# Optimization experiments

Measured on AMD Instinct MI355X. Metric: run time of the kernel, lower is better.

Reference implementation:

```python
import jax, jax.numpy as jnp
import numpy as np

N_NODES = 50000
N_EDGES = 640000
DIM = 128
N_LAYERS = 4
K_MAX = 4


def setup_inputs() -> dict:
    key = jax.random.key(0)
    k1, k2, k3, k4, k5, k6 = jax.random.split(key, 6)
    x = jax.random.normal(k1, (N_NODES, DIM), dtype=jnp.float32)
    edge_index = jax.random.randint(k2, (2, N_EDGES), 0, N_NODES, dtype=jnp.int32)
    edge_attr = jax.random.randint(k3, (N_EDGES,), 1, K_MAX + 1, dtype=jnp.int32)  # hop k in [1, k_max]
    W = jax.random.normal(k4, (N_LAYERS, DIM, DIM), dtype=jnp.float32) * 0.05
    b = jax.random.normal(k5, (N_LAYERS, DIM), dtype=jnp.float32) * 0.01
    alpha = jax.random.normal(k6, (N_LAYERS, K_MAX), dtype=jnp.float32)
    return {"x": x, "edge_index": edge_index, "edge_attr": edge_attr,
            "W": W, "b": b, "alpha": alpha}


def reference(x, edge_index, edge_attr, W, b, alpha):
    # SP-GCN stage: per-hop GCN convs with shared per-layer weight W[t],
    # combined with softmax(alpha[t]) hop weights, residual + ReLU + L2 norm.
    N, D = x.shape
    L, K = alpha.shape
    src, dst = edge_index[0], edge_index[1]
    k_idx = edge_attr - 1                              # [E] in [0, K)

    # Per-(node, hop) in-degree with self-loop (+1), as in gcn_norm per k-subgraph.
    seg = dst * K + k_idx
    ones = jnp.ones(src.shape[0], dtype=x.dtype)
    deg = jax.ops.segment_sum(ones, seg, num_segments=N * K).reshape(N, K) + 1.0  # [N, K]
    dinv = jax.lax.rsqrt(deg)
    # symmetric norm per edge within its hop-k subgraph
    norm_e = dinv[src, k_idx] * dinv[dst, k_idx]       # [E]

    for t in range(L):
        a = jax.nn.softmax(alpha[t])                   # [K] hop weights
        h = x @ W[t]                                   # [N, D]
        # sum_k alpha_k * conv_k fused: per-edge weight alpha[k_e] * norm_e
        msg = (a[k_idx] * norm_e)[:, None] * h[src]    # [E, D]
        agg = jax.ops.segment_sum(msg, dst, num_segments=N)
        # self-loop contributions: sum_k alpha_k / deg[n, k]
        self_coef = jnp.sum(a[None, :] / deg, axis=1)  # [N]
        out = agg + self_coef[:, None] * h + b[t]
        x = x + jax.nn.relu(out)
        # F.normalize(p=2, dim=-1), eps=1e-12
        nrm = jnp.maximum(jnp.linalg.norm(x, axis=-1, keepdims=True), 1e-12)
        x = x / nrm
    return x
```

## Files before the change

kernel.cpp:

```cpp
#include <hip/hip_runtime.h>
#include <hip/hip_fp16.h>
#include <math.h>

#define DIM 128
#define KH 4

typedef unsigned int uint;
typedef unsigned short ushort;
using short8v = __attribute__((ext_vector_type(8))) short;
using f32x4 = __attribute__((ext_vector_type(4))) float;

__device__ __forceinline__ uint f2bf(float f) {
  uint u = __float_as_uint(f);
  return (u + 0x7fffu + ((u >> 16) & 1u)) >> 16;
}
__device__ __forceinline__ float bf2f(uint u) { return __uint_as_float(u << 16); }
__device__ __forceinline__ float bflo(uint u) { return __uint_as_float(u << 16); }
__device__ __forceinline__ float bfhi(uint u) { return __uint_as_float(u & 0xffff0000u); }

__global__ __launch_bounds__(256) void k_init(const float4* __restrict__ xin,
                                              float4* __restrict__ X4,
                                              uint* __restrict__ Xhi,
                                              uint* __restrict__ Xlo,
                                              uint* __restrict__ degpack,
                                              int n4, int N) {
  int i = blockIdx.x * 256 + threadIdx.x;
  if (i < n4) {
    float4 v = xin[i];
    X4[i] = v;
    uint h0 = f2bf(v.x), h1 = f2bf(v.y), h2 = f2bf(v.z), h3 = f2bf(v.w);
    Xhi[i * 2 + 0] = h0 | (h1 << 16);
    Xhi[i * 2 + 1] = h2 | (h3 << 16);
    uint l0 = f2bf(v.x - bf2f(h0)), l1 = f2bf(v.y - bf2f(h1));
    uint l2 = f2bf(v.z - bf2f(h2)), l3 = f2bf(v.w - bf2f(h3));
    Xlo[i * 2 + 0] = l0 | (l1 << 16);
    Xlo[i * 2 + 1] = l2 | (l3 << 16);
  }
  if (i < N) degpack[i] = 0;
}

__global__ __launch_bounds__(256) void k_wprep(const float* __restrict__ W,
                                               short* __restrict__ Whi,
                                               short* __restrict__ Wlo, int total) {
  int idx = blockIdx.x * 256 + threadIdx.x;
  if (idx >= total) return;
  int l = idx >> 14;
  int rem = idx & 16383;
  int k = rem >> 7;
  int n = rem & 127;
  float w = W[idx];
  uint h = f2bf(w);
  uint lo = f2bf(w - bf2f(h));
  size_t o = (size_t)l * 16384 + (size_t)n * 128 + k;
  Whi[o] = (short)h;
  Wlo[o] = (short)lo;
}

__global__ __launch_bounds__(256) void k_count(const int* __restrict__ ei,
                                               const int* __restrict__ attr,
                                               uint* __restrict__ degpack, int E) {
  int e = blockIdx.x * 256 + threadIdx.x;
  if (e >= E) return;
  int dst = ei[E + e];
  int k = attr[e] - 1;
  atomicAdd(&degpack[dst], 1u << (k * 8));
}

__global__ __launch_bounds__(256) void k_scan1(const uint* __restrict__ degpack,
                                               int* __restrict__ off,
                                               int* __restrict__ bsum, int n) {
  __shared__ int s[256];
  int t = threadIdx.x;
  int i = blockIdx.x * 256 + t;
  int v = 0;
  if (i < n) {
    uint w = degpack[i];
    v = (w & 0xff) + ((w >> 8) & 0xff) + ((w >> 16) & 0xff) + (w >> 24);
  }
  s[t] = v;
  __syncthreads();
  for (int d = 1; d < 256; d <<= 1) {
    int u = (t >= d) ? s[t - d] : 0;
    __syncthreads();
    s[t] += u;
    __syncthreads();
  }
  if (i < n) off[i] = s[t] - v;
  if (t == 255) bsum[blockIdx.x] = s[255];
}

__global__ __launch_bounds__(256) void k_scan2(const int* __restrict__ bsum,
                                               int* __restrict__ bex, int nb) {
  __shared__ int s[256];
  int t = threadIdx.x;
  int v = (t < nb) ? bsum[t] : 0;
  s[t] = v;
  __syncthreads();
  for (int d = 1; d < 256; d <<= 1) {
    int u = (t >= d) ? s[t - d] : 0;
    __syncthreads();
    s[t] += u;
    __syncthreads();
  }
  if (t < nb) bex[t] = s[t] - v;
}

__global__ __launch_bounds__(256) void k_scan3(int* __restrict__ off,
                                               const int* __restrict__ bex,
                                               const uint* __restrict__ degpack,
                                               int* __restrict__ cursor4,
                                               float* __restrict__ dinv, int n) {
  int i = blockIdx.x * 256 + threadIdx.x;
  if (i >= n) return;
  int o = off[i] + bex[blockIdx.x];
  off[i] = o;
  uint w = degpack[i];
  int b0 = w & 0xff, b1 = (w >> 8) & 0xff, b2 = (w >> 16) & 0xff, b3 = w >> 24;
  int4 c;
  c.x = o;
  c.y = o + b0;
  c.z = o + b0 + b1;
  c.w = o + b0 + b1 + b2;
  *(int4*)&cursor4[i * 4] = c;
  float4 dv;
  dv.x = rsqrtf((float)b0 + 1.0f);
  dv.y = rsqrtf((float)b1 + 1.0f);
  dv.z = rsqrtf((float)b2 + 1.0f);
  dv.w = rsqrtf((float)b3 + 1.0f);
  *(float4*)&dinv[i * 4] = dv;
}

__global__ __launch_bounds__(256) void k_scatter(const int* __restrict__ ei,
                                                 const int* __restrict__ attr,
                                                 const float* __restrict__ dinv,
                                                 int* __restrict__ cursor4,
                                                 uint* __restrict__ srcnm, int E) {
  int e = blockIdx.x * 256 + threadIdx.x;
  if (e >= E) return;
  int src = ei[e];
  int dst = ei[E + e];
  int k = attr[e] - 1;
  float nm = dinv[src * KH + k] * dinv[dst * KH + k];
  ushort h = __half_as_ushort(__float2half(nm));
  int pos = atomicAdd(&cursor4[dst * KH + k], 1);
  srcnm[pos] = (uint)src | ((uint)h << 16);
}

__global__ __launch_bounds__(512) void k_gemm(const uint* __restrict__ Xhi,
                                              const uint* __restrict__ Xlo,
                                              const short* __restrict__ Whi,
                                              const short* __restrict__ Wlo,
                                              ushort* __restrict__ Hb16, int N) {
  __shared__ __align__(16) short xs_hi[64 * 128];
  __shared__ __align__(16) short xs_lo[64 * 128];
  int t = threadIdx.x;
  int r0 = blockIdx.x * 64;

#pragma unroll
  for (int i = 0; i < 2; ++i) {
    int fi = i * 512 + t;
    int row = fi >> 4, kq = fi & 15;
    int rg = r0 + row;
    if (rg >= N) rg = N - 1;
    int swz = kq ^ (row & 7);
    *(uint4*)&xs_hi[row * 128 + swz * 8] = *(const uint4*)&Xhi[(size_t)rg * 64 + kq * 4];
    *(uint4*)&xs_lo[row * 128 + swz * 8] = *(const uint4*)&Xlo[(size_t)rg * 64 + kq * 4];
  }
  __syncthreads();

  int wid = t >> 6, lane = t & 63;
  int wrow = wid & 1, wcol = wid >> 1;
  int lr = lane & 15, lk = lane >> 4;

  f32x4 acc[2][2];
#pragma unroll
  for (int a = 0; a < 2; ++a)
#pragma unroll
    for (int c = 0; c < 2; ++c) acc[a][c] = (f32x4){0.f, 0.f, 0.f, 0.f};

#pragma unroll
  for (int ks = 0; ks < 4; ++ks) {
    int k0 = ks * 32 + lk * 8;
    short8v ah[2], al[2];
#pragma unroll
    for (int rt = 0; rt < 2; ++rt) {
      int r = wrow * 32 + rt * 16 + lr;
      int slot = (k0 >> 3) ^ (r & 7);
      ah[rt] = *(short8v*)&xs_hi[r * 128 + slot * 8];
      al[rt] = *(short8v*)&xs_lo[r * 128 + slot * 8];
    }
    short8v bh[2], bl[2];
#pragma unroll
    for (int ct = 0; ct < 2; ++ct) {
      int col = wcol * 32 + ct * 16 + lr;
      bh[ct] = *(const short8v*)&Whi[(size_t)col * 128 + k0];
      bl[ct] = *(const short8v*)&Wlo[(size_t)col * 128 + k0];
    }
#pragma unroll
    for (int rt = 0; rt < 2; ++rt)
#pragma unroll
      for (int ct = 0; ct < 2; ++ct) {
        acc[rt][ct] = __builtin_amdgcn_mfma_f32_16x16x32_bf16(ah[rt], bh[ct], acc[rt][ct], 0, 0, 0);
        acc[rt][ct] = __builtin_amdgcn_mfma_f32_16x16x32_bf16(al[rt], bh[ct], acc[rt][ct], 0, 0, 0);
        acc[rt][ct] = __builtin_amdgcn_mfma_f32_16x16x32_bf16(ah[rt], bl[ct], acc[rt][ct], 0, 0, 0);
      }
  }

#pragma unroll
  for (int rt = 0; rt < 2; ++rt)
#pragma unroll
    for (int ct = 0; ct < 2; ++ct) {
      int col = wcol * 32 + ct * 16 + lr;
#pragma unroll
      for (int i = 0; i < 4; ++i) {
        int row = r0 + wrow * 32 + rt * 16 + lk * 4 + i;
        if (row < N) Hb16[(size_t)row * 128 + col] = (ushort)f2bf(acc[rt][ct][i]);
      }
    }
}

__global__ __launch_bounds__(256) void k_agg(const int* __restrict__ off,
                                             const uint* __restrict__ degpack,
                                             const uint* __restrict__ srcnm,
                                             const float* __restrict__ dinv,
                                             const uint* __restrict__ Hb,
                                             const float* __restrict__ bias,
                                             const float* __restrict__ alpha,
                                             float* __restrict__ X,
                                             uint* __restrict__ Xhi,
                                             uint* __restrict__ Xlo, int N) {
  int wid = threadIdx.x >> 6;
  int lane = threadIdx.x & 63;
  int n = blockIdx.x * 4 + wid;
  if (n >= N) return;

  float a0 = alpha[0], a1 = alpha[1], a2 = alpha[2], a3 = alpha[3];
  float m = fmaxf(fmaxf(a0, a1), fmaxf(a2, a3));
  a0 = __expf(a0 - m); a1 = __expf(a1 - m); a2 = __expf(a2 - m); a3 = __expf(a3 - m);
  float is = 1.0f / (a0 + a1 + a2 + a3);
  a0 *= is; a1 *= is; a2 *= is; a3 *= is;

  uint w = degpack[n];
  int b0 = w & 0xff, b1 = (w >> 8) & 0xff, b2 = (w >> 16) & 0xff, b3 = (int)(w >> 24);
  int e0 = off[n];
  int e1 = e0 + b0 + b1 + b2 + b3;
  int k1 = e0 + b0, k2 = k1 + b1, k3 = k2 + b2;

  float accx = 0.f, accy = 0.f;

  for (int base = e0; base < e1; base += 64) {
    int cnt = min(64, e1 - base);
    int sofs = 0;
    float wc = 0.f;
    if (lane < cnt) {
      uint v = srcnm[base + lane];
      int pos = base + lane;
      int k = (pos >= k1) + (pos >= k2) + (pos >= k3);
      float ak = (k == 0) ? a0 : (k == 1) ? a1 : (k == 2) ? a2 : a3;
      wc = ak * __half2float(__ushort_as_half((ushort)(v >> 16)));
      sofs = (int)(v & 0xFFFFu) << 6;
    }
    int j = 0;
    for (; j + 4 <= cnt; j += 4) {
      int s0 = __shfl(sofs, j),     s1 = __shfl(sofs, j + 1);
      int s2 = __shfl(sofs, j + 2), s3 = __shfl(sofs, j + 3);
      float w0 = __shfl(wc, j),     w1 = __shfl(wc, j + 1);
      float w2 = __shfl(wc, j + 2), w3 = __shfl(wc, j + 3);
      uint u0 = Hb[s0 + lane];
      uint u1 = Hb[s1 + lane];
      uint u2 = Hb[s2 + lane];
      uint u3 = Hb[s3 + lane];
      accx = fmaf(w0, bflo(u0), accx); accy = fmaf(w0, bfhi(u0), accy);
      accx = fmaf(w1, bflo(u1), accx); accy = fmaf(w1, bfhi(u1), accy);
      accx = fmaf(w2, bflo(u2), accx); accy = fmaf(w2, bfhi(u2), accy);
      accx = fmaf(w3, bflo(u3), accx); accy = fmaf(w3, bfhi(u3), accy);
    }
    for (; j < cnt; ++j) {
      int sj = __shfl(sofs, j);
      float wj = __shfl(wc, j);
      uint uj = Hb[sj + lane];
      accx = fmaf(wj, bflo(uj), accx);
      accy = fmaf(wj, bfhi(uj), accy);
    }
  }

  float4 dv = *(const float4*)&dinv[n * 4];
  float sc = a0 * dv.x * dv.x + a1 * dv.y * dv.y + a2 * dv.z * dv.z + a3 * dv.w * dv.w;

  uint un = Hb[(size_t)n * 64 + lane];
  float2 bb = ((const float2*)bias)[lane];
  float2 xo = ((const float2*)X)[(size_t)n * 64 + lane];
  float o0 = accx + sc * bflo(un) + bb.x;
  float o1 = accy + sc * bfhi(un) + bb.y;
  float x0 = xo.x + fmaxf(o0, 0.f);
  float x1 = xo.y + fmaxf(o1, 0.f);

  float ss = x0 * x0 + x1 * x1;
#pragma unroll
  for (int d = 32; d; d >>= 1) ss += __shfl_xor(ss, d);
  float nrm = fmaxf(sqrtf(ss), 1e-12f);
  float inv = 1.0f / nrm;
  float y0 = x0 * inv, y1 = x1 * inv;
  ((float2*)X)[(size_t)n * 64 + lane] = make_float2(y0, y1);

  uint h0 = f2bf(y0), h1 = f2bf(y1);
  Xhi[(size_t)n * 64 + lane] = h0 | (h1 << 16);
  uint l0 = f2bf(y0 - bf2f(h0)), l1 = f2bf(y1 - bf2f(h1));
  Xlo[(size_t)n * 64 + lane] = l0 | (l1 << 16);
}

extern "C" void kernel_launch(void* const* d_in, const int* in_sizes, int n_in,
                              void* d_out, int out_size, void* d_ws, size_t ws_size,
                              hipStream_t stream) {
  const float* x = (const float*)d_in[0];
  const int* ei = (const int*)d_in[1];
  const int* attr = (const int*)d_in[2];
  const float* W = (const float*)d_in[3];
  const float* b = (const float*)d_in[4];
  const float* alpha = (const float*)d_in[5];
  float* X = (float*)d_out;

  int N = in_sizes[0] / DIM;
  int E = in_sizes[1] / 2;
  int L = in_sizes[3] / (DIM * DIM);

  char* base = (char*)d_ws;
  size_t ofs = 0;
  auto carve = [&](size_t bytes) -> void* {
    void* p = base + ofs;
    ofs = (ofs + bytes + 255) & ~(size_t)255;
    return p;
  };
  int* off = (int*)carve((size_t)(N + 1) * 4);
  int* cursor4 = (int*)carve((size_t)N * KH * 4);
  uint* degpack = (uint*)carve((size_t)N * 4);
  float* dinv = (float*)carve((size_t)N * KH * 4);
  int* bsum = (int*)carve(256 * 4);
  int* bex = (int*)carve(256 * 4);
  uint* srcnm = (uint*)carve((size_t)E * 4);
  uint* Hb = (uint*)carve((size_t)N * 64 * 4);
  uint* Xhi = (uint*)carve((size_t)N * 64 * 4);
  uint* Xlo = (uint*)carve((size_t)N * 64 * 4);
  short* Whi = (short*)carve((size_t)L * DIM * DIM * 2);
  short* Wlo = (short*)carve((size_t)L * DIM * DIM * 2);

  int n4 = N * DIM / 4;
  int nb = (N + 255) / 256;
  int wtot = L * DIM * DIM;

  k_init<<<(n4 + 255) / 256, 256, 0, stream>>>((const float4*)x, (float4*)X,
                                               Xhi, Xlo, degpack, n4, N);
  k_count<<<(E + 255) / 256, 256, 0, stream>>>(ei, attr, degpack, E);
  k_scan1<<<nb, 256, 0, stream>>>(degpack, off, bsum, N);
  k_scan2<<<1, 256, 0, stream>>>(bsum, bex, nb);
  k_scan3<<<nb, 256, 0, stream>>>(off, bex, degpack, cursor4, dinv, N);
  k_scatter<<<(E + 255) / 256, 256, 0, stream>>>(ei, attr, dinv, cursor4, srcnm, E);
  k_wprep<<<(wtot + 255) / 256, 256, 0, stream>>>(W, Whi, Wlo, wtot);

  for (int t = 0; t < L; ++t) {
    k_gemm<<<(N + 63) / 64, 512, 0, stream>>>(Xhi, Xlo,
                                              Whi + (size_t)t * DIM * DIM,
                                              Wlo + (size_t)t * DIM * DIM,
                                              (ushort*)Hb, N);
    k_agg<<<(N + 3) / 4, 256, 0, stream>>>(off, degpack, srcnm, dinv, Hb,
                                           b + (size_t)t * DIM, alpha + (size_t)t * KH,
                                           X, Xhi, Xlo, N);
  }
}
```

Before: 318.4 us.

## Fuse aggregation, GEMM and normalization into one per-layer kernel

Reorders each layer to aggregate first and multiply second, (A·X)·W instead of A·(X·W). Aggregation, the split-bf16 MFMA GEMM and the residual/ReLU/L2-normalize now run in one kernel per layer that keeps the intermediate rows in shared memory, with fp16 copies of X used for the neighbor gathers. Setup kernels are also merged (init+count, scan3+weight prep), a memset is used, and X buffers ping-pong between layers. This removes the Hb round trip to global memory and one launch per layer. In exchange, 512-thread blocks each gather 64 rows serially (8 per wave), which may lower latency hiding, and fp16 gathers change numerical precision.

```diff
diff --git a/kernel.cpp b/kernel.cpp
--- a/kernel.cpp
+++ b/kernel.cpp
@@ -15,55 +15,21 @@
   return (u + 0x7fffu + ((u >> 16) & 1u)) >> 16;
 }
 __device__ __forceinline__ float bf2f(uint u) { return __uint_as_float(u << 16); }
-__device__ __forceinline__ float bflo(uint u) { return __uint_as_float(u << 16); }
-__device__ __forceinline__ float bfhi(uint u) { return __uint_as_float(u & 0xffff0000u); }
-
-__global__ __launch_bounds__(256) void k_init(const float4* __restrict__ xin,
-                                              float4* __restrict__ X4,
-                                              uint* __restrict__ Xhi,
-                                              uint* __restrict__ Xlo,
-                                              uint* __restrict__ degpack,
-                                              int n4, int N) {
+
+__global__ __launch_bounds__(256) void k_init_count(
+    const float2* __restrict__ xin, __half2* __restrict__ Xf16,
+    const int* __restrict__ ei, const int* __restrict__ attr,
+    uint* __restrict__ degpack, int n2, int E) {
   int i = blockIdx.x * 256 + threadIdx.x;
-  if (i < n4) {
-    float4 v = xin[i];
-    X4[i] = v;
-    uint h0 = f2bf(v.x), h1 = f2bf(v.y), h2 = f2bf(v.z), h3 = f2bf(v.w);
-    Xhi[i * 2 + 0] = h0 | (h1 << 16);
-    Xhi[i * 2 + 1] = h2 | (h3 << 16);
-    uint l0 = f2bf(v.x - bf2f(h0)), l1 = f2bf(v.y - bf2f(h1));
-    uint l2 = f2bf(v.z - bf2f(h2)), l3 = f2bf(v.w - bf2f(h3));
-    Xlo[i * 2 + 0] = l0 | (l1 << 16);
-    Xlo[i * 2 + 1] = l2 | (l3 << 16);
-  }
-  if (i < N) degpack[i] = 0;
-}
-
-__global__ __launch_bounds__(256) void k_wprep(const float* __restrict__ W,
-                                               short* __restrict__ Whi,
-                                               short* __restrict__ Wlo, int total) {
-  int idx = blockIdx.x * 256 + threadIdx.x;
-  if (idx >= total) return;
-  int l = idx >> 14;
-  int rem = idx & 16383;
-  int k = rem >> 7;
-  int n = rem & 127;
-  float w = W[idx];
-  uint h = f2bf(w);
-  uint lo = f2bf(w - bf2f(h));
-  size_t o = (size_t)l * 16384 + (size_t)n * 128 + k;
-  Whi[o] = (short)h;
-  Wlo[o] = (short)lo;
-}
-
-__global__ __launch_bounds__(256) void k_count(const int* __restrict__ ei,
-                                               const int* __restrict__ attr,
-                                               uint* __restrict__ degpack, int E) {
-  int e = blockIdx.x * 256 + threadIdx.x;
-  if (e >= E) return;
-  int dst = ei[E + e];
-  int k = attr[e] - 1;
-  atomicAdd(&degpack[dst], 1u << (k * 8));
+  if (i < n2) {
+    float2 v = xin[i];
+    Xf16[i] = __floats2half2_rn(v.x, v.y);
+  }
+  if (i < E) {
+    int dst = ei[E + i];
+    int k = attr[i] - 1;
+    atomicAdd(&degpack[dst], 1u << (k * 8));
+  }
 }
 
 __global__ __launch_bounds__(256) void k_scan1(const uint* __restrict__ degpack,
@@ -105,29 +71,45 @@
   if (t < nb) bex[t] = s[t] - v;
 }
 
-__global__ __launch_bounds__(256) void k_scan3(int* __restrict__ off,
-                                               const int* __restrict__ bex,
-                                               const uint* __restrict__ degpack,
-                                               int* __restrict__ cursor4,
-                                               float* __restrict__ dinv, int n) {
+__global__ __launch_bounds__(256) void k_scan3w(int* __restrict__ off,
+                                                const int* __restrict__ bex,
+                                                const uint* __restrict__ degpack,
+                                                int* __restrict__ cursor4,
+                                                float* __restrict__ dinv, int n,
+                                                const float* __restrict__ W,
+                                                short* __restrict__ Whi,
+                                                short* __restrict__ Wlo, int wtot) {
   int i = blockIdx.x * 256 + threadIdx.x;
-  if (i >= n) return;
-  int o = off[i] + bex[blockIdx.x];
-  off[i] = o;
-  uint w = degpack[i];
-  int b0 = w & 0xff, b1 = (w >> 8) & 0xff, b2 = (w >> 16) & 0xff, b3 = w >> 24;
-  int4 c;
-  c.x = o;
-  c.y = o + b0;
-  c.z = o + b0 + b1;
-  c.w = o + b0 + b1 + b2;
-  *(int4*)&cursor4[i * 4] = c;
-  float4 dv;
-  dv.x = rsqrtf((float)b0 + 1.0f);
-  dv.y = rsqrtf((float)b1 + 1.0f);
-  dv.z = rsqrtf((float)b2 + 1.0f);
-  dv.w = rsqrtf((float)b3 + 1.0f);
-  *(float4*)&dinv[i * 4] = dv;
+  if (i < n) {
+    int o = off[i] + bex[blockIdx.x];
+    off[i] = o;
+    uint w = degpack[i];
+    int b0 = w & 0xff, b1 = (w >> 8) & 0xff, b2 = (w >> 16) & 0xff, b3 = w >> 24;
+    int4 c;
+    c.x = o;
+    c.y = o + b0;
+    c.z = o + b0 + b1;
+    c.w = o + b0 + b1 + b2;
+    *(int4*)&cursor4[i * 4] = c;
+    float4 dv;
+    dv.x = rsqrtf((float)b0 + 1.0f);
+    dv.y = rsqrtf((float)b1 + 1.0f);
+    dv.z = rsqrtf((float)b2 + 1.0f);
+    dv.w = rsqrtf((float)b3 + 1.0f);
+    *(float4*)&dinv[i * 4] = dv;
+  }
+  if (i < wtot) {
+    int l = i >> 14;
+    int rem = i & 16383;
+    int k = rem >> 7;
+    int ncol = rem & 127;
+    float w = W[i];
+    uint h = f2bf(w);
+    uint lo = f2bf(w - bf2f(h));
+    size_t o = (size_t)l * 16384 + (size_t)ncol * 128 + k;
+    Whi[o] = (short)h;
+    Wlo[o] = (short)lo;
+  }
 }
 
 __global__ __launch_bounds__(256) void k_scatter(const int* __restrict__ ei,
@@ -146,32 +128,100 @@
   srcnm[pos] = (uint)src | ((uint)h << 16);
 }
 
-__global__ __launch_bounds__(512) void k_gemm(const uint* __restrict__ Xhi,
-                                              const uint* __restrict__ Xlo,
-                                              const short* __restrict__ Whi,
-                                              const short* __restrict__ Wlo,
-                                              ushort* __restrict__ Hb16, int N) {
-  __shared__ __align__(16) short xs_hi[64 * 128];
-  __shared__ __align__(16) short xs_lo[64 * 128];
+__device__ __forceinline__ void split8(f32x4 va, f32x4 vb, short8v& h, short8v& l) {
+#pragma unroll
+  for (int j = 0; j < 8; ++j) {
+    float v = (j < 4) ? va[j] : vb[j - 4];
+    uint hh = f2bf(v);
+    h[j] = (short)hh;
+    l[j] = (short)f2bf(v - bf2f(hh));
+  }
+}
+
+__global__ __launch_bounds__(512) void k_layer(
+    const int* __restrict__ off, const uint* __restrict__ degpack,
+    const uint* __restrict__ srcnm, const float* __restrict__ dinv,
+    const float2* __restrict__ Xin,
+    const __half2* __restrict__ Xf16_in,
+    const short* __restrict__ Whi, const short* __restrict__ Wlo,
+    const float* __restrict__ bias, const float* __restrict__ alpha,
+    float2* __restrict__ Xout,
+    __half2* __restrict__ Xf16_out,
+    int N) {
+  __shared__ __align__(16) char aggb[64 * 512];
   int t = threadIdx.x;
+  int wid = t >> 6, lane = t & 63;
   int r0 = blockIdx.x * 64;
 
-#pragma unroll
-  for (int i = 0; i < 2; ++i) {
-    int fi = i * 512 + t;
-    int row = fi >> 4, kq = fi & 15;
-    int rg = r0 + row;
-    if (rg >= N) rg = N - 1;
-    int swz = kq ^ (row & 7);
-    *(uint4*)&xs_hi[row * 128 + swz * 8] = *(const uint4*)&Xhi[(size_t)rg * 64 + kq * 4];
-    *(uint4*)&xs_lo[row * 128 + swz * 8] = *(const uint4*)&Xlo[(size_t)rg * 64 + kq * 4];
-  }
-  __syncthreads();
-
-  int wid = t >> 6, lane = t & 63;
+  float a0 = alpha[0], a1 = alpha[1], a2 = alpha[2], a3 = alpha[3];
+  float m = fmaxf(fmaxf(a0, a1), fmaxf(a2, a3));
+  a0 = __expf(a0 - m); a1 = __expf(a1 - m); a2 = __expf(a2 - m); a3 = __expf(a3 - m);
+  float is = 1.0f / (a0 + a1 + a2 + a3);
+  a0 *= is; a1 *= is; a2 *= is; a3 *= is;
+
+  float2 xsave[8];
+
+  for (int ni = 0; ni < 8; ++ni) {
+    int row = wid * 8 + ni;
+    int n = r0 + row;
+    if (n >= N) n = N - 1;
+    uint w = degpack[n];
+    int b0 = w & 0xff, b1 = (w >> 8) & 0xff, b2 = (w >> 16) & 0xff, b3 = (int)(w >> 24);
+    int e0 = off[n];
+    int e1 = e0 + b0 + b1 + b2 + b3;
+    int k1 = e0 + b0, k2 = k1 + b1, k3 = k2 + b2;
+    float accx = 0.f, accy = 0.f;
+
+    for (int base = e0; base < e1; base += 64) {
+      int cnt = min(64, e1 - base);
+      int sofs = 0;
+      float wc = 0.f;
+      if (lane < cnt) {
+        uint v = srcnm[base + lane];
+        int pos = base + lane;
+        int k = (pos >= k1) + (pos >= k2) + (pos >= k3);
+        float ak = (k == 0) ? a0 : (k == 1) ? a1 : (k == 2) ? a2 : a3;
+        wc = ak * __half2float(__ushort_as_half((ushort)(v >> 16)));
+        sofs = (int)(v & 0xFFFFu) << 6;
+      }
+      int j = 0;
+      for (; j + 4 <= cnt; j += 4) {
+        int s0 = __shfl(sofs, j),     s1 = __shfl(sofs, j + 1);
+        int s2 = __shfl(sofs, j + 2), s3 = __shfl(sofs, j + 3);
+        float w0 = __shfl(wc, j),     w1 = __shfl(wc, j + 1);
+        float w2 = __shfl(wc, j + 2), w3 = __shfl(wc, j + 3);
+        float2 f0 = __half22float2(Xf16_in[s0 + lane]);
+        float2 f1 = __half22float2(Xf16_in[s1 + lane]);
+        float2 f2 = __half22float2(Xf16_in[s2 + lane]);
+        float2 f3 = __half22float2(Xf16_in[s3 + lane]);
+        accx = fmaf(w0, f0.x, accx); accy = fmaf(w0, f0.y, accy);
+        accx = fmaf(w1, f1.x, accx); accy = fmaf(w1, f1.y, accy);
+        accx = fmaf(w2, f2.x, accx); accy = fmaf(w2, f2.y, accy);
+        accx = fmaf(w3, f3.x, accx); accy = fmaf(w3, f3.y, accy);
+      }
+      for (; j < cnt; ++j) {
+        int sj = __shfl(sofs, j);
+        float wj = __shfl(wc, j);
+        float2 fj = __half22float2(Xf16_in[sj + lane]);
+        accx = fmaf(wj, fj.x, accx);
+        accy = fmaf(wj, fj.y, accy);
+      }
+    }
+
+    float4 dv = *(const float4*)&dinv[n * 4];
+    float sc = a0 * dv.x * dv.x + a1 * dv.y * dv.y + a2 * dv.z * dv.z + a3 * dv.w * dv.w;
+    float2 xn = Xin[(size_t)n * 64 + lane];
+    xsave[ni] = xn;
+    accx = fmaf(sc, xn.x, accx);
+    accy = fmaf(sc, xn.y, accy);
+
+    int slot = (lane >> 1) ^ ((row & 7) << 1);
+    *(float2*)(aggb + row * 512 + slot * 16 + (lane & 1) * 8) = make_float2(accx, accy);
+  }
+  __syncthreads();
+
   int wrow = wid & 1, wcol = wid >> 1;
   int lr = lane & 15, lk = lane >> 4;
-
   f32x4 acc[2][2];
 #pragma unroll
   for (int a = 0; a < 2; ++a)
@@ -185,9 +235,10 @@
 #pragma unroll
     for (int rt = 0; rt < 2; ++rt) {
       int r = wrow * 32 + rt * 16 + lr;
-      int slot = (k0 >> 3) ^ (r & 7);
-      ah[rt] = *(short8v*)&xs_hi[r * 128 + slot * 8];
-      al[rt] = *(short8v*)&xs_lo[r * 128 + slot * 8];
+      int s0 = (k0 >> 2) ^ ((r & 7) << 1);
+      f32x4 va = *(f32x4*)(aggb + r * 512 + s0 * 16);
+      f32x4 vb = *(f32x4*)(aggb + r * 512 + s0 * 16 + 16);
+      split8(va, vb, ah[rt], al[rt]);
     }
     short8v bh[2], bl[2];
 #pragma unroll
@@ -205,6 +256,7 @@
         acc[rt][ct] = __builtin_amdgcn_mfma_f32_16x16x32_bf16(ah[rt], bl[ct], acc[rt][ct], 0, 0, 0);
       }
   }
+  __syncthreads();
 
 #pragma unroll
   for (int rt = 0; rt < 2; ++rt)
@@ -213,100 +265,30 @@
       int col = wcol * 32 + ct * 16 + lr;
 #pragma unroll
       for (int i = 0; i < 4; ++i) {
-        int row = r0 + wrow * 32 + rt * 16 + lk * 4 + i;
-        if (row < N) Hb16[(size_t)row * 128 + col] = (ushort)f2bf(acc[rt][ct][i]);
+        int row = wrow * 32 + rt * 16 + lk * 4 + i;
+        int slot = (col >> 2) ^ ((row & 7) << 1);
+        *(float*)(aggb + row * 512 + slot * 16 + (col & 3) * 4) = acc[rt][ct][i];
       }
     }
-}
-
-__global__ __launch_bounds__(256) void k_agg(const int* __restrict__ off,
-                                             const uint* __restrict__ degpack,
-                                             const uint* __restrict__ srcnm,
-                                             const float* __restrict__ dinv,
-                                             const uint* __restrict__ Hb,
-                                             const float* __restrict__ bias,
-                                             const float* __restrict__ alpha,
-                                             float* __restrict__ X,
-                                             uint* __restrict__ Xhi,
-                                             uint* __restrict__ Xlo, int N) {
-  int wid = threadIdx.x >> 6;
-  int lane = threadIdx.x & 63;
-  int n = blockIdx.x * 4 + wid;
-  if (n >= N) return;
-
-  float a0 = alpha[0], a1 = alpha[1], a2 = alpha[2], a3 = alpha[3];
-  float m = fmaxf(fmaxf(a0, a1), fmaxf(a2, a3));
-  a0 = __expf(a0 - m); a1 = __expf(a1 - m); a2 = __expf(a2 - m); a3 = __expf(a3 - m);
-  float is = 1.0f / (a0 + a1 + a2 + a3);
-  a0 *= is; a1 *= is; a2 *= is; a3 *= is;
-
-  uint w = degpack[n];
-  int b0 = w & 0xff, b1 = (w >> 8) & 0xff, b2 = (w >> 16) & 0xff, b3 = (int)(w >> 24);
-  int e0 = off[n];
-  int e1 = e0 + b0 + b1 + b2 + b3;
-  int k1 = e0 + b0, k2 = k1 + b1, k3 = k2 + b2;
-
-  float accx = 0.f, accy = 0.f;
-
-  for (int base = e0; base < e1; base += 64) {
-    int cnt = min(64, e1 - base);
-    int sofs = 0;
-    float wc = 0.f;
-    if (lane < cnt) {
-      uint v = srcnm[base + lane];
-      int pos = base + lane;
-      int k = (pos >= k1) + (pos >= k2) + (pos >= k3);
-      float ak = (k == 0) ? a0 : (k == 1) ? a1 : (k == 2) ? a2 : a3;
-      wc = ak * __half2float(__ushort_as_half((ushort)(v >> 16)));
-      sofs = (int)(v & 0xFFFFu) << 6;
-    }
-    int j = 0;
-    for (; j + 4 <= cnt; j += 4) {
-      int s0 = __shfl(sofs, j),     s1 = __shfl(sofs, j + 1);
-      int s2 = __shfl(sofs, j + 2), s3 = __shfl(sofs, j + 3);
-      float w0 = __shfl(wc, j),     w1 = __shfl(wc, j + 1);
-      float w2 = __shfl(wc, j + 2), w3 = __shfl(wc, j + 3);
-      uint u0 = Hb[s0 + lane];
-      uint u1 = Hb[s1 + lane];
-      uint u2 = Hb[s2 + lane];
-      uint u3 = Hb[s3 + lane];
-      accx = fmaf(w0, bflo(u0), accx); accy = fmaf(w0, bfhi(u0), accy);
-      accx = fmaf(w1, bflo(u1), accx); accy = fmaf(w1, bfhi(u1), accy);
-      accx = fmaf(w2, bflo(u2), accx); accy = fmaf(w2, bfhi(u2), accy);
-      accx = fmaf(w3, bflo(u3), accx); accy = fmaf(w3, bfhi(u3), accy);
-    }
-    for (; j < cnt; ++j) {
-      int sj = __shfl(sofs, j);
-      float wj = __shfl(wc, j);
-      uint uj = Hb[sj + lane];
-      accx = fmaf(wj, bflo(uj), accx);
-      accy = fmaf(wj, bfhi(uj), accy);
-    }
-  }
-
-  float4 dv = *(const float4*)&dinv[n * 4];
-  float sc = a0 * dv.x * dv.x + a1 * dv.y * dv.y + a2 * dv.z * dv.z + a3 * dv.w * dv.w;
-
-  uint un = Hb[(size_t)n * 64 + lane];
+  __syncthreads();
+
   float2 bb = ((const float2*)bias)[lane];
-  float2 xo = ((const float2*)X)[(size_t)n * 64 + lane];
-  float o0 = accx + sc * bflo(un) + bb.x;
-  float o1 = accy + sc * bfhi(un) + bb.y;
-  float x0 = xo.x + fmaxf(o0, 0.f);
-  float x1 = xo.y + fmaxf(o1, 0.f);
-
-  float ss = x0 * x0 + x1 * x1;
-#pragma unroll
-  for (int d = 32; d; d >>= 1) ss += __shfl_xor(ss, d);
-  float nrm = fmaxf(sqrtf(ss), 1e-12f);
-  float inv = 1.0f / nrm;
-  float y0 = x0 * inv, y1 = x1 * inv;
-  ((float2*)X)[(size_t)n * 64 + lane] = make_float2(y0, y1);
-
-  uint h0 = f2bf(y0), h1 = f2bf(y1);
-  Xhi[(size_t)n * 64 + lane] = h0 | (h1 << 16);
-  uint l0 = f2bf(y0 - bf2f(h0)), l1 = f2bf(y1 - bf2f(h1));
-  Xlo[(size_t)n * 64 + lane] = l0 | (l1 << 16);
+  for (int ni = 0; ni < 8; ++ni) {
+    int row = wid * 8 + ni;
+    int n = r0 + row;
+    if (n >= N) continue;
+    int slot = (lane >> 1) ^ ((row & 7) << 1);
+    float2 o = *(float2*)(aggb + row * 512 + slot * 16 + (lane & 1) * 8);
+    float x0 = xsave[ni].x + fmaxf(o.x + bb.x, 0.f);
+    float x1 = xsave[ni].y + fmaxf(o.y + bb.y, 0.f);
+    float ss = x0 * x0 + x1 * x1;
+#pragma unroll
+    for (int d = 32; d; d >>= 1) ss += __shfl_xor(ss, d);
+    float inv = 1.0f / fmaxf(sqrtf(ss), 1e-12f);
+    float y0 = x0 * inv, y1 = x1 * inv;
+    Xout[(size_t)n * 64 + lane] = make_float2(y0, y1);
+    Xf16_out[(size_t)n * 64 + lane] = __floats2half2_rn(y0, y1);
+  }
 }
 
 extern "C" void kernel_launch(void* const* d_in, const int* in_sizes, int n_in,
@@ -338,32 +320,40 @@
   int* bsum = (int*)carve(256 * 4);
   int* bex = (int*)carve(256 * 4);
   uint* srcnm = (uint*)carve((size_t)E * 4);
-  uint* Hb = (uint*)carve((size_t)N * 64 * 4);
-  uint* Xhi = (uint*)carve((size_t)N * 64 * 4);
-  uint* Xlo = (uint*)carve((size_t)N * 64 * 4);
+  float* XP0 = (float*)carve((size_t)N * DIM * 4);
+  float* XP1 = (float*)carve((size_t)N * DIM * 4);
+  __half2* Xf16A = (__half2*)carve((size_t)N * 64 * 4);
+  __half2* Xf16B = (__half2*)carve((size_t)N * 64 * 4);
   short* Whi = (short*)carve((size_t)L * DIM * DIM * 2);
   short* Wlo = (short*)carve((size_t)L * DIM * DIM * 2);
 
-  int n4 = N * DIM / 4;
+  int n2 = N * DIM / 2;
   int nb = (N + 255) / 256;
   int wtot = L * DIM * DIM;
-
-  k_init<<<(n4 + 255) / 256, 256, 0, stream>>>((const float4*)x, (float4*)X,
-                                               Xhi, Xlo, degpack, n4, N);
-  k_count<<<(E + 255) / 256, 256, 0, stream>>>(ei, attr, degpack, E);
+  int nb64 = (N + 63) / 64;
+  int gmax = (wtot > N) ? wtot : N;
+
+  hipMemsetAsync(degpack, 0, (size_t)N * 4, stream);
+  k_init_count<<<(n2 + 255) / 256, 256, 0, stream>>>((const float2*)x, Xf16A,
+                                                     ei, attr, degpack, n2, E);
   k_scan1<<<nb, 256, 0, stream>>>(degpack, off, bsum, N);
   k_scan2<<<1, 256, 0, stream>>>(bsum, bex, nb);
-  k_scan3<<<nb, 256, 0, stream>>>(off, bex, degpack, cursor4, dinv, N);
+  k_scan3w<<<(gmax + 255) / 256, 256, 0, stream>>>(off, bex, degpack, cursor4, dinv, N,
+                                                   W, Whi, Wlo, wtot);
   k_scatter<<<(E + 255) / 256, 256, 0, stream>>>(ei, attr, dinv, cursor4, srcnm, E);
-  k_wprep<<<(wtot + 255) / 256, 256, 0, stream>>>(W, Whi, Wlo, wtot);
 
   for (int t = 0; t < L; ++t) {
-    k_gemm<<<(N + 63) / 64, 512, 0, stream>>>(Xhi, Xlo,
-                                              Whi + (size_t)t * DIM * DIM,
-                                              Wlo + (size_t)t * DIM * DIM,
-                                              (ushort*)Hb, N);
-    k_agg<<<(N + 3) / 4, 256, 0, stream>>>(off, degpack, srcnm, dinv, Hb,
-                                           b + (size_t)t * DIM, alpha + (size_t)t * KH,
-                                           X, Xhi, Xlo, N);
-  }
-}
+    const float2* Xin = (t == 0) ? (const float2*)x
+                                 : (const float2*)((t & 1) ? XP0 : XP1);
+    float2* Xout = (t == L - 1) ? (float2*)X
+                                : (float2*)((t & 1) ? XP1 : XP0);
+    const __half2* Fin = (t & 1) ? Xf16B : Xf16A;
+    __half2* Fout = (t & 1) ? Xf16A : Xf16B;
+    k_layer<<<nb64, 512, 0, stream>>>(off, degpack, srcnm, dinv,
+                                      Xin, Fin,
+                                      Whi + (size_t)t * DIM * DIM,
+                                      Wlo + (size_t)t * DIM * DIM,
+                                      b + (size_t)t * DIM, alpha + (size_t)t * KH,
+                                      Xout, Fout, N);
+  }
+}
```

Result: slower. 365.6 us (+14.8%).
